# Kernel optimization log

Measured on AMD Instinct MI355X. Metric: run time of the kernel, lower is better.

## Reference

```python
import jax, jax.numpy as jnp
import numpy as np
from jax import lax

RHO = 1.0
L = 50

def _pbc_index(rho=RHO, L=L):
    # S = {(m,n) | |mn| <= rho*L//2, |m|<=L//2, |n|<=L//2}; rho*L//2 == 25.0 here
    thr = (rho * L) // 2
    idx = [(m, n)
           for m in range(-L // 2, L // 2 + 1)
           for n in range(-L // 2, L // 2 + 1)
           if abs(m * n) <= thr]
    return np.asarray(idx, dtype=np.int32)  # [T, 2], T = 449


def setup_inputs() -> dict:
    key = jax.random.key(0)
    k1, k2, k3, k4 = jax.random.split(key, 4)
    B, S, Nmodes = 8, 16384, 2
    T = _pbc_index().shape[0]  # 449
    return {
        "E_real": jax.random.normal(k1, (B, S, Nmodes), dtype=jnp.float32),
        "E_imag": jax.random.normal(k2, (B, S, Nmodes), dtype=jnp.float32),
        "C_real": jax.random.normal(k3, (4, T), dtype=jnp.float32) * 0.01,
        "C_imag": jax.random.normal(k4, (4, T), dtype=jnp.float32) * 0.01,
    }


def reference(E_real, E_imag, C_real, C_imag):
    idx = _pbc_index()
    m = jnp.asarray(idx[:, 0])
    n = jnp.asarray(idx[:, 1])
    E = E_real + 1j * E_imag                 # [B, S, 2] complex64
    C = (C_real + 1j * C_imag)[0]            # task_info=None -> row 0, [T]

    # O_k,i = E_k,i + sum_{m,n} (E_{k+n,i} E*_{k+m+n,i} + E_{k+n,-i} E*_{k+m+n,-i}) E_{k+m,i} C_{m,n}
    def body(acc, term):
        mi, ni, ci = term
        A = jnp.roll(E, ni, axis=-2) * jnp.conj(jnp.roll(E, mi + ni, axis=-2))
        A = A + jnp.roll(A, 1, axis=-1)      # cross-polarization term (Nmodes=2)
        return acc + A * jnp.roll(E, mi, axis=-2) * ci, None

    acc, _ = lax.scan(body, jnp.zeros_like(E), (m, n, C))
    Eo = E + acc                             # P = 1 (task_info=None), sqrt(P)**3 = 1
    return Eo[..., L:-L, :]                  # drop overlaps: [B, S-2L, 2]
```

## Files before the change

kernel.cpp:

```cpp
#include <hip/hip_runtime.h>


typedef float v2f __attribute__((ext_vector_type(2)));
typedef float v4f __attribute__((ext_vector_type(4)));

#define S_LEN 16384
#define SOUT  16284
#define BLK   512
#define NOUT  256
#define NE    356
#define NE2   178
#define ND    307
#define ND_AL 308
#define NDP   154

constexpr int LIMS[26] = {25,25,12,8,6,5,4,3,3,2,2,2,2,
                          1,1,1,1,1,1,1,1,1,1,1,1,1};
constexpr int TS[51] = {
      0,  3,  6,  9, 12, 15, 18, 21, 24, 27, 30, 33, 36,
     39, 44, 49, 54, 59, 66, 73, 82, 93,106,123,148,199,
    250,301,326,343,356,367,376,383,390,395,400,405,410,
    413,416,419,422,425,428,431,434,437,440,443,446};

template<int M>
__device__ __forceinline__ void convM(
    const float2* __restrict__ sDm, const v4f* __restrict__ sEp,
    int o0, const float* __restrict__ Cr0, const float* __restrict__ Ci0,
    float4& acc)
{
    constexpr int lim = LIMS[M];
    constexpr int tp  = TS[25 + M];
    constexpr int tn  = TS[25 - M];
    constexpr int A   = 25 + lim;

    v2f SxP0 = {0.f,0.f}, SyP0 = {0.f,0.f}, SxP1 = {0.f,0.f}, SyP1 = {0.f,0.f};
    v2f SxN0 = {0.f,0.f}, SyN0 = {0.f,0.f}, SxN1 = {0.f,0.f}, SyN1 = {0.f,0.f};

#define TAP(dconst, dd)                                                     \
    {                                                                       \
        const int d_ = (dconst);                                            \
        if (A - d_ >= 0 && A - d_ <= 2*lim) {                               \
            const float cx = Cr0[tp + A - d_], cy = Ci0[tp + A - d_];       \
            SxP0 += cx * (dd);  SyP0 += cy * (dd);                          \
        }                                                                   \
        if (A + 1 - d_ >= 0 && A + 1 - d_ <= 2*lim) {                       \
            const float cx = Cr0[tp + A+1-d_], cy = Ci0[tp + A+1-d_];       \
            SxP1 += cx * (dd);  SyP1 += cy * (dd);                          \
        }                                                                   \
        if (A + M - d_ >= 0 && A + M - d_ <= 2*lim) {                       \
            const float cx = Cr0[tn + A+M-d_], cy = Ci0[tn + A+M-d_];       \
            SxN0 += cx * (dd);  SyN0 += cy * (dd);                          \
        }                                                                   \
        if (A + M + 1 - d_ >= 0 && A + M + 1 - d_ <= 2*lim) {               \
            const float cx = Cr0[tn + A+M+1-d_], cy = Ci0[tn + A+M+1-d_];   \
            SxN1 += cx * (dd);  SyN1 += cy * (dd);                          \
        }                                                                   \
    }

    if constexpr (M < 2*lim + 4) {
        constexpr int dlo = (25 - lim) & ~1;
        constexpr int dhi = 26 + lim + M;
        constexpr int NP  = (dhi - dlo) / 2 + 1;
        #pragma unroll
        for (int p = 0; p < NP; ++p) {
            const int d0 = dlo + 2*p;
            v4f w = *reinterpret_cast<const v4f*>(&sDm[o0 + d0]);
            TAP(d0,     w.xy)
            TAP(d0 + 1, w.zw)
        }
    } else {
        {
            constexpr int dlo = (25 - lim) & ~1;
            constexpr int dhi = 26 + lim;
            constexpr int NP  = (dhi - dlo) / 2 + 1;
            #pragma unroll
            for (int p = 0; p < NP; ++p) {
                const int d0 = dlo + 2*p;
                v4f w = *reinterpret_cast<const v4f*>(&sDm[o0 + d0]);
                #pragma unroll
                for (int e = 0; e < 2; ++e) {
                    const int d = d0 + e;
                    const v2f dd = e ? w.zw : w.xy;
                    if (A - d >= 0 && A - d <= 2*lim) {
                        const float cx = Cr0[tp + A - d], cy = Ci0[tp + A - d];
                        SxP0 += cx * dd;  SyP0 += cy * dd;
                    }
                    if (A + 1 - d >= 0 && A + 1 - d <= 2*lim) {
                        const float cx = Cr0[tp + A+1-d], cy = Ci0[tp + A+1-d];
                        SxP1 += cx * dd;  SyP1 += cy * dd;
                    }
                }
            }
        }
        {
            constexpr int dlo = (25 + M - lim) & ~1;
            constexpr int dhi = 26 + M + lim;
            constexpr int NP  = (dhi - dlo) / 2 + 1;
            #pragma unroll
            for (int p = 0; p < NP; ++p) {
                const int d0 = dlo + 2*p;
                v4f w = *reinterpret_cast<const v4f*>(&sDm[o0 + d0]);
                #pragma unroll
                for (int e = 0; e < 2; ++e) {
                    const int d = d0 + e;
                    const v2f dd = e ? w.zw : w.xy;
                    if (A + M - d >= 0 && A + M - d <= 2*lim) {
                        const float cx = Cr0[tn + A+M-d], cy = Ci0[tn + A+M-d];
                        SxN0 += cx * dd;  SyN0 += cy * dd;
                    }
                    if (A + M + 1 - d >= 0 && A + M + 1 - d <= 2*lim) {
                        const float cx = Cr0[tn + A+M+1-d], cy = Ci0[tn + A+M+1-d];
                        SxN1 += cx * dd;  SyN1 += cy * dd;
                    }
                }
            }
        }
    }
#undef TAP

    const float s0pr = SxP0.x - SyP0.y, s0pi = SxP0.y + SyP0.x;
    const float s1pr = SxP1.x - SyP1.y, s1pi = SxP1.y + SyP1.x;
    const float s0nr = SxN0.x + SyN0.y, s0ni = SyN0.x - SxN0.y;
    const float s1nr = SxN1.x + SyN1.y, s1ni = SyN1.x - SxN1.y;

    const int t = o0 >> 1;
    v4f ep0, ep1, en0, en1;
    if constexpr ((M & 1) == 0) {
        ep0 = sEp[t + (50 - M)/2];
        ep1 = sEp[t + (50 - M)/2 + NE2];
        en0 = sEp[t + (50 + M)/2];
        en1 = sEp[t + (50 + M)/2 + NE2];
    } else {
        ep0 = sEp[t + (49 - M)/2 + NE2];
        ep1 = sEp[t + (51 - M)/2];
        en0 = sEp[t + (49 + M)/2 + NE2];
        en1 = sEp[t + (51 + M)/2];
    }
    acc.x += s0pr*ep0.x - s0pi*ep0.y + s0nr*en0.x - s0ni*en0.y;
    acc.y += s0pr*ep0.z - s0pi*ep0.w + s0nr*en0.z - s0ni*en0.w;
    acc.z += s1pr*ep1.x - s1pi*ep1.y + s1nr*en1.x - s1ni*en1.y;
    acc.w += s1pr*ep1.z - s1pi*ep1.w + s1nr*en1.z - s1ni*en1.w;
}

__device__ __forceinline__ void conv0(
    const float* __restrict__ sD0p, const v4f* __restrict__ sEp,
    int o0, const float* __restrict__ Cr0, const float* __restrict__ Ci0,
    float4& acc)
{
    v2f s0 = {0.f, 0.f}, s1 = {0.f, 0.f};
    #pragma unroll
    for (int p = 0; p < 13; ++p) {
        const int d0 = 4*p;
        v4f w = *reinterpret_cast<const v4f*>(&sD0p[o0 + d0]);
        #pragma unroll
        for (int e = 0; e < 4; ++e) {
            const int d = d0 + e;
            const float dv = (e == 0) ? w.x : (e == 1) ? w.y : (e == 2) ? w.z : w.w;
            if (50 - d >= 0) {
                v2f cv = { Cr0[199 + 50 - d], Ci0[199 + 50 - d] };
                s0 += dv * cv;
            }
            if (51 - d >= 0 && 51 - d <= 50) {
                v2f cv = { Cr0[199 + 51 - d], Ci0[199 + 51 - d] };
                s1 += dv * cv;
            }
        }
    }
    const int t = o0 >> 1;
    v4f e0 = sEp[t + 25];
    v4f e1 = sEp[t + 25 + NE2];
    acc.x += s0.x*e0.x - s0.y*e0.y;
    acc.y += s0.x*e0.z - s0.y*e0.w;
    acc.z += s1.x*e1.x - s1.y*e1.y;
    acc.w += s1.x*e1.z - s1.y*e1.w;
}

__global__ __launch_bounds__(BLK, 4) void pbc_kernel(
    const float* __restrict__ Er, const float* __restrict__ Ei,
    const float* __restrict__ Cr, const float* __restrict__ Ci,
    float* __restrict__ out)
{
    __shared__ __align__(16) v4f    sEp[NE];
    __shared__ __align__(16) float2 sD[25][ND_AL];
    __shared__ __align__(16) float  sD0[ND_AL];
    __shared__ __align__(16) float4 sAcc[4][128];

    const int b   = blockIdx.y;
    const int k0  = blockIdx.x * NOUT;
    const int tid = threadIdx.x;

    const float* erb = Er + (size_t)b * (S_LEN * 2);
    const float* eib = Ei + (size_t)b * (S_LEN * 2);
    if (tid < NE2) {
        const int i  = tid;
        const int kg = k0 + 2 * i;
        v4f rr = {0.f,0.f,0.f,0.f}, ii = {0.f,0.f,0.f,0.f};
        if (kg < S_LEN) {
            rr = *reinterpret_cast<const v4f*>(erb + 2 * kg);
            ii = *reinterpret_cast<const v4f*>(eib + 2 * kg);
        }
        sEp[i]       = (v4f){rr.x, ii.x, rr.y, ii.y};
        sEp[i + NE2] = (v4f){rr.z, ii.z, rr.w, ii.w};
    }
    __syncthreads();

    if (tid < NDP) {
        const int xp = tid;
        v4f a0 = sEp[xp + 12 + NE2];
        v4f a1 = sEp[xp + 13];
        float d0 = a0.x*a0.x + a0.y*a0.y + a0.z*a0.z + a0.w*a0.w;
        float d1 = a1.x*a1.x + a1.y*a1.y + a1.z*a1.z + a1.w*a1.w;
        *reinterpret_cast<float2*>(&sD0[2 * xp]) = make_float2(d0, d1);
    }
    for (int idx = tid; idx < 25 * NDP; idx += BLK) {
        const int m1 = idx / NDP;
        const int xp = idx - m1 * NDP;
        const int m  = m1 + 1;
        v4f a0 = sEp[xp + 12 + NE2];
        v4f a1 = sEp[xp + 13];
        const int sb  = 2 * xp + 25 - m;
        const int ib0 = (sb >> 1) + (sb & 1) * NE2;
        const int sb1 = sb + 1;
        const int ib1 = (sb1 >> 1) + (sb1 & 1) * NE2;
        v4f b0 = sEp[ib0], b1 = sEp[ib1];
        float gr0 = a0.x*b0.x + a0.y*b0.y + a0.z*b0.z + a0.w*b0.w;
        float gi0 = a0.y*b0.x - a0.x*b0.y + a0.w*b0.z - a0.z*b0.w;
        float gr1 = a1.x*b1.x + a1.y*b1.y + a1.z*b1.z + a1.w*b1.w;
        float gi1 = a1.y*b1.x - a1.x*b1.y + a1.w*b1.z - a1.z*b1.w;
        *reinterpret_cast<v4f*>(&sD[m1][2 * xp]) = (v4f){gr0, gi0, gr1, gi1};
    }
    __syncthreads();

    const int g  = tid >> 7;
    const int t  = tid & 127;
    const int o0 = 2 * t;

    float4 acc = make_float4(0.f, 0.f, 0.f, 0.f);
    if (g == 0) {
        convM<1>(sD[0],   sEp, o0, Cr, Ci, acc);
        convM<13>(sD[12], sEp, o0, Cr, Ci, acc);
        convM<14>(sD[13], sEp, o0, Cr, Ci, acc);
        convM<15>(sD[14], sEp, o0, Cr, Ci, acc);
        convM<16>(sD[15], sEp, o0, Cr, Ci, acc);
        convM<17>(sD[16], sEp, o0, Cr, Ci, acc);
    } else if (g == 1) {
        convM<2>(sD[1],   sEp, o0, Cr, Ci, acc);
        convM<4>(sD[3],   sEp, o0, Cr, Ci, acc);
        convM<7>(sD[6],   sEp, o0, Cr, Ci, acc);
        convM<9>(sD[8],   sEp, o0, Cr, Ci, acc);
        convM<18>(sD[17], sEp, o0, Cr, Ci, acc);
        convM<19>(sD[18], sEp, o0, Cr, Ci, acc);
    } else if (g == 2) {
        conv0(sD0, sEp, o0, Cr, Ci, acc);
        convM<3>(sD[2],   sEp, o0, Cr, Ci, acc);
        convM<8>(sD[7],   sEp, o0, Cr, Ci, acc);
        convM<10>(sD[9],  sEp, o0, Cr, Ci, acc);
        convM<12>(sD[11], sEp, o0, Cr, Ci, acc);
        convM<20>(sD[19], sEp, o0, Cr, Ci, acc);
    } else {
        convM<5>(sD[4],   sEp, o0, Cr, Ci, acc);
        convM<6>(sD[5],   sEp, o0, Cr, Ci, acc);
        convM<11>(sD[10], sEp, o0, Cr, Ci, acc);
        convM<21>(sD[20], sEp, o0, Cr, Ci, acc);
        convM<22>(sD[21], sEp, o0, Cr, Ci, acc);
        convM<23>(sD[22], sEp, o0, Cr, Ci, acc);
        convM<24>(sD[23], sEp, o0, Cr, Ci, acc);
        convM<25>(sD[24], sEp, o0, Cr, Ci, acc);
    }
    sAcc[g][t] = acc;
    __syncthreads();

    if (tid < 128) {
        const int tt = tid;
        const int oo = 2 * tt;
        const int ko = k0 + oo;
        if (ko < SOUT) {
            float4 p0 = sAcc[0][tt], p1 = sAcc[1][tt];
            float4 p2 = sAcc[2][tt], p3 = sAcc[3][tt];
            v4f e0 = sEp[tt + 25];
            v4f e1 = sEp[tt + 25 + NE2];
            float4 o;
            o.x = e0.x + p0.x + p1.x + p2.x + p3.x;
            o.y = e0.z + p0.y + p1.y + p2.y + p3.y;
            o.z = e1.x + p0.z + p1.z + p2.z + p3.z;
            o.w = e1.z + p0.w + p1.w + p2.w + p3.w;
            *reinterpret_cast<float4*>(out + ((size_t)b * SOUT + ko) * 2) = o;
        }
    }
}

extern "C" void kernel_launch(void* const* d_in, const int* in_sizes, int n_in,
                              void* d_out, int out_size, void* d_ws, size_t ws_size,
                              hipStream_t stream) {
    const float* Er = (const float*)d_in[0];
    const float* Ei = (const float*)d_in[1];
    const float* Cr = (const float*)d_in[2];
    const float* Ci = (const float*)d_in[3];
    float* out = (float*)d_out;

    dim3 grid((SOUT + NOUT - 1) / NOUT, 8);
    pbc_kernel<<<grid, BLK, 0, stream>>>(Er, Ei, Cr, Ci, out);
}
```

Measured before the change: 17.34 us.

## Register-block four outputs per thread, store intermediates as bf16, regroup warps

Each thread now computes four consecutive outputs instead of two, so every shared-memory load of the intermediate products feeds four accumulators. The per-m intermediate products are packed to bf16 pairs, which halves LDS footprint and read bandwidth. The m-values are redistributed over eight 64-thread groups, with a seven-way cross-group reduction at the end. This trades lower LDS traffic for more registers per thread and reduced precision of the intermediate terms, which may affect accuracy.

```diff
diff --git a/kernel.cpp b/kernel.cpp
--- a/kernel.cpp
+++ b/kernel.cpp
@@ -22,157 +22,156 @@
     250,301,326,343,356,367,376,383,390,395,400,405,410,
     413,416,419,422,425,428,431,434,437,440,443,446};
 
+__device__ __forceinline__ uint32_t pack_bf(float re, float im) {
+    uint32_t r;
+    asm("v_cvt_pk_bf16_f32 %0, %1, %2" : "=v"(r) : "v"(re), "v"(im));
+    return r;
+}
+__device__ __forceinline__ v2f unpack_bf(uint32_t u) {
+    union { uint32_t i; float f; } lo, hi;
+    lo.i = u << 16;
+    hi.i = u & 0xFFFF0000u;
+    return (v2f){lo.f, hi.f};
+}
+
 template<int M>
-__device__ __forceinline__ void convM(
-    const float2* __restrict__ sDm, const v4f* __restrict__ sEp,
+__device__ __forceinline__ void convM4(
+    const uint32_t* __restrict__ sDm, const v4f* __restrict__ sEp,
     int o0, const float* __restrict__ Cr0, const float* __restrict__ Ci0,
-    float4& acc)
+    float4& acc01, float4& acc23)
 {
     constexpr int lim = LIMS[M];
     constexpr int tp  = TS[25 + M];
     constexpr int tn  = TS[25 - M];
     constexpr int A   = 25 + lim;
 
-    v2f SxP0 = {0.f,0.f}, SyP0 = {0.f,0.f}, SxP1 = {0.f,0.f}, SyP1 = {0.f,0.f};
-    v2f SxN0 = {0.f,0.f}, SyN0 = {0.f,0.f}, SxN1 = {0.f,0.f}, SyN1 = {0.f,0.f};
-
-#define TAP(dconst, dd)                                                     \
+    v2f SxP[4] = {{0.f,0.f},{0.f,0.f},{0.f,0.f},{0.f,0.f}};
+    v2f SyP[4] = {{0.f,0.f},{0.f,0.f},{0.f,0.f},{0.f,0.f}};
+    v2f SxN[4] = {{0.f,0.f},{0.f,0.f},{0.f,0.f},{0.f,0.f}};
+    v2f SyN[4] = {{0.f,0.f},{0.f,0.f},{0.f,0.f},{0.f,0.f}};
+
+#define TAP4(d_, dd)                                                        \
+    { _Pragma("unroll")                                                     \
+      for (int r = 0; r < 4; ++r) {                                         \
+        if (A + r - (d_) >= 0 && A + r - (d_) <= 2*lim) {                   \
+            const float cx = Cr0[tp + A + r - (d_)];                        \
+            const float cy = Ci0[tp + A + r - (d_)];                        \
+            SxP[r] += cx * (dd);  SyP[r] += cy * (dd);                      \
+        }                                                                   \
+        if (A + M + r - (d_) >= 0 && A + M + r - (d_) <= 2*lim) {           \
+            const float cx = Cr0[tn + A + M + r - (d_)];                    \
+            const float cy = Ci0[tn + A + M + r - (d_)];                    \
+            SxN[r] += cx * (dd);  SyN[r] += cy * (dd);                      \
+        }                                                                   \
+      } }
+#define TAP4P(d_, dd)                                                       \
+    { _Pragma("unroll")                                                     \
+      for (int r = 0; r < 4; ++r) {                                         \
+        if (A + r - (d_) >= 0 && A + r - (d_) <= 2*lim) {                   \
+            const float cx = Cr0[tp + A + r - (d_)];                        \
+            const float cy = Ci0[tp + A + r - (d_)];                        \
+            SxP[r] += cx * (dd);  SyP[r] += cy * (dd);                      \
+        }                                                                   \
+      } }
+#define TAP4N(d_, dd)                                                       \
+    { _Pragma("unroll")                                                     \
+      for (int r = 0; r < 4; ++r) {                                         \
+        if (A + M + r - (d_) >= 0 && A + M + r - (d_) <= 2*lim) {           \
+            const float cx = Cr0[tn + A + M + r - (d_)];                    \
+            const float cy = Ci0[tn + A + M + r - (d_)];                    \
+            SxN[r] += cx * (dd);  SyN[r] += cy * (dd);                      \
+        }                                                                   \
+      } }
+#define QUAD(d0_, TAPM)                                                     \
     {                                                                       \
-        const int d_ = (dconst);                                            \
-        if (A - d_ >= 0 && A - d_ <= 2*lim) {                               \
-            const float cx = Cr0[tp + A - d_], cy = Ci0[tp + A - d_];       \
-            SxP0 += cx * (dd);  SyP0 += cy * (dd);                          \
-        }                                                                   \
-        if (A + 1 - d_ >= 0 && A + 1 - d_ <= 2*lim) {                       \
-            const float cx = Cr0[tp + A+1-d_], cy = Ci0[tp + A+1-d_];       \
-            SxP1 += cx * (dd);  SyP1 += cy * (dd);                          \
-        }                                                                   \
-        if (A + M - d_ >= 0 && A + M - d_ <= 2*lim) {                       \
-            const float cx = Cr0[tn + A+M-d_], cy = Ci0[tn + A+M-d_];       \
-            SxN0 += cx * (dd);  SyN0 += cy * (dd);                          \
-        }                                                                   \
-        if (A + M + 1 - d_ >= 0 && A + M + 1 - d_ <= 2*lim) {               \
-            const float cx = Cr0[tn + A+M+1-d_], cy = Ci0[tn + A+M+1-d_];   \
-            SxN1 += cx * (dd);  SyN1 += cy * (dd);                          \
-        }                                                                   \
+        uint4 u = *reinterpret_cast<const uint4*>(&sDm[o0 + (d0_)]);        \
+        TAPM((d0_) + 0, unpack_bf(u.x))                                     \
+        TAPM((d0_) + 1, unpack_bf(u.y))                                     \
+        TAPM((d0_) + 2, unpack_bf(u.z))                                     \
+        TAPM((d0_) + 3, unpack_bf(u.w))                                     \
     }
 
     if constexpr (M < 2*lim + 4) {
-        constexpr int dlo = (25 - lim) & ~1;
-        constexpr int dhi = 26 + lim + M;
-        constexpr int NP  = (dhi - dlo) / 2 + 1;
+        constexpr int dlo = (25 - lim) & ~3;
+        constexpr int dhi = 28 + lim + M;
+        constexpr int NQ  = (dhi - dlo) / 4 + 1;
         #pragma unroll
-        for (int p = 0; p < NP; ++p) {
-            const int d0 = dlo + 2*p;
-            v4f w = *reinterpret_cast<const v4f*>(&sDm[o0 + d0]);
-            TAP(d0,     w.xy)
-            TAP(d0 + 1, w.zw)
-        }
+        for (int q = 0; q < NQ; ++q)
+            QUAD(dlo + 4*q, TAP4)
     } else {
         {
-            constexpr int dlo = (25 - lim) & ~1;
-            constexpr int dhi = 26 + lim;
-            constexpr int NP  = (dhi - dlo) / 2 + 1;
+            constexpr int dlo = (25 - lim) & ~3;
+            constexpr int dhi = 28 + lim;
+            constexpr int NQ  = (dhi - dlo) / 4 + 1;
             #pragma unroll
-            for (int p = 0; p < NP; ++p) {
-                const int d0 = dlo + 2*p;
-                v4f w = *reinterpret_cast<const v4f*>(&sDm[o0 + d0]);
-                #pragma unroll
-                for (int e = 0; e < 2; ++e) {
-                    const int d = d0 + e;
-                    const v2f dd = e ? w.zw : w.xy;
-                    if (A - d >= 0 && A - d <= 2*lim) {
-                        const float cx = Cr0[tp + A - d], cy = Ci0[tp + A - d];
-                        SxP0 += cx * dd;  SyP0 += cy * dd;
-                    }
-                    if (A + 1 - d >= 0 && A + 1 - d <= 2*lim) {
-                        const float cx = Cr0[tp + A+1-d], cy = Ci0[tp + A+1-d];
-                        SxP1 += cx * dd;  SyP1 += cy * dd;
-                    }
-                }
-            }
+            for (int q = 0; q < NQ; ++q)
+                QUAD(dlo + 4*q, TAP4P)
         }
         {
-            constexpr int dlo = (25 + M - lim) & ~1;
-            constexpr int dhi = 26 + M + lim;
-            constexpr int NP  = (dhi - dlo) / 2 + 1;
+            constexpr int dlo = (25 + M - lim) & ~3;
+            constexpr int dhi = 28 + M + lim;
+            constexpr int NQ  = (dhi - dlo) / 4 + 1;
             #pragma unroll
-            for (int p = 0; p < NP; ++p) {
-                const int d0 = dlo + 2*p;
-                v4f w = *reinterpret_cast<const v4f*>(&sDm[o0 + d0]);
-                #pragma unroll
-                for (int e = 0; e < 2; ++e) {
-                    const int d = d0 + e;
-                    const v2f dd = e ? w.zw : w.xy;
-                    if (A + M - d >= 0 && A + M - d <= 2*lim) {
-                        const float cx = Cr0[tn + A+M-d], cy = Ci0[tn + A+M-d];
-                        SxN0 += cx * dd;  SyN0 += cy * dd;
-                    }
-                    if (A + M + 1 - d >= 0 && A + M + 1 - d <= 2*lim) {
-                        const float cx = Cr0[tn + A+M+1-d], cy = Ci0[tn + A+M+1-d];
-                        SxN1 += cx * dd;  SyN1 += cy * dd;
-                    }
-                }
-            }
-        }
-    }
-#undef TAP
-
-    const float s0pr = SxP0.x - SyP0.y, s0pi = SxP0.y + SyP0.x;
-    const float s1pr = SxP1.x - SyP1.y, s1pi = SxP1.y + SyP1.x;
-    const float s0nr = SxN0.x + SyN0.y, s0ni = SyN0.x - SxN0.y;
-    const float s1nr = SxN1.x + SyN1.y, s1ni = SyN1.x - SxN1.y;
-
-    const int t = o0 >> 1;
-    v4f ep0, ep1, en0, en1;
-    if constexpr ((M & 1) == 0) {
-        ep0 = sEp[t + (50 - M)/2];
-        ep1 = sEp[t + (50 - M)/2 + NE2];
-        en0 = sEp[t + (50 + M)/2];
-        en1 = sEp[t + (50 + M)/2 + NE2];
-    } else {
-        ep0 = sEp[t + (49 - M)/2 + NE2];
-        ep1 = sEp[t + (51 - M)/2];
-        en0 = sEp[t + (49 + M)/2 + NE2];
-        en1 = sEp[t + (51 + M)/2];
-    }
-    acc.x += s0pr*ep0.x - s0pi*ep0.y + s0nr*en0.x - s0ni*en0.y;
-    acc.y += s0pr*ep0.z - s0pi*ep0.w + s0nr*en0.z - s0ni*en0.w;
-    acc.z += s1pr*ep1.x - s1pi*ep1.y + s1nr*en1.x - s1ni*en1.y;
-    acc.w += s1pr*ep1.z - s1pi*ep1.w + s1nr*en1.z - s1ni*en1.w;
-}
-
-__device__ __forceinline__ void conv0(
+            for (int q = 0; q < NQ; ++q)
+                QUAD(dlo + 4*q, TAP4N)
+        }
+    }
+#undef QUAD
+#undef TAP4
+#undef TAP4P
+#undef TAP4N
+
+    #pragma unroll
+    for (int r = 0; r < 4; ++r) {
+        const float spr = SxP[r].x - SyP[r].y, spi = SxP[r].y + SyP[r].x;
+        const float snr = SxN[r].x + SyN[r].y, sni = SyN[r].x - SxN[r].y;
+        const int sp = o0 + 50 + r - M;
+        const int sn = o0 + 50 + r + M;
+        v4f ep = sEp[(sp >> 1) + ((sp & 1) ? NE2 : 0)];
+        v4f en = sEp[(sn >> 1) + ((sn & 1) ? NE2 : 0)];
+        const float c0 = spr*ep.x - spi*ep.y + snr*en.x - sni*en.y;
+        const float c1 = spr*ep.z - spi*ep.w + snr*en.z - sni*en.w;
+        if      (r == 0) { acc01.x += c0; acc01.y += c1; }
+        else if (r == 1) { acc01.z += c0; acc01.w += c1; }
+        else if (r == 2) { acc23.x += c0; acc23.y += c1; }
+        else             { acc23.z += c0; acc23.w += c1; }
+    }
+}
+
+__device__ __forceinline__ void conv04(
     const float* __restrict__ sD0p, const v4f* __restrict__ sEp,
     int o0, const float* __restrict__ Cr0, const float* __restrict__ Ci0,
-    float4& acc)
+    float4& acc01, float4& acc23)
 {
-    v2f s0 = {0.f, 0.f}, s1 = {0.f, 0.f};
+    v2f s[4] = {{0.f,0.f},{0.f,0.f},{0.f,0.f},{0.f,0.f}};
     #pragma unroll
-    for (int p = 0; p < 13; ++p) {
-        const int d0 = 4*p;
+    for (int q = 0; q < 14; ++q) {
+        const int d0 = 4*q;
         v4f w = *reinterpret_cast<const v4f*>(&sD0p[o0 + d0]);
         #pragma unroll
         for (int e = 0; e < 4; ++e) {
             const int d = d0 + e;
-            const float dv = (e == 0) ? w.x : (e == 1) ? w.y : (e == 2) ? w.z : w.w;
-            if (50 - d >= 0) {
-                v2f cv = { Cr0[199 + 50 - d], Ci0[199 + 50 - d] };
-                s0 += dv * cv;
+            const float dv = (e==0) ? w.x : (e==1) ? w.y : (e==2) ? w.z : w.w;
+            #pragma unroll
+            for (int r = 0; r < 4; ++r) {
+                if (50 + r - d >= 0 && 50 + r - d <= 50) {
+                    v2f cv = { Cr0[199 + 50 + r - d], Ci0[199 + 50 + r - d] };
+                    s[r] += dv * cv;
+                }
             }
-            if (51 - d >= 0 && 51 - d <= 50) {
-                v2f cv = { Cr0[199 + 51 - d], Ci0[199 + 51 - d] };
-                s1 += dv * cv;
-            }
-        }
-    }
-    const int t = o0 >> 1;
-    v4f e0 = sEp[t + 25];
-    v4f e1 = sEp[t + 25 + NE2];
-    acc.x += s0.x*e0.x - s0.y*e0.y;
-    acc.y += s0.x*e0.z - s0.y*e0.w;
-    acc.z += s1.x*e1.x - s1.y*e1.y;
-    acc.w += s1.x*e1.z - s1.y*e1.w;
+        }
+    }
+    #pragma unroll
+    for (int r = 0; r < 4; ++r) {
+        const int sp = o0 + 50 + r;
+        v4f e = sEp[(sp >> 1) + ((sp & 1) ? NE2 : 0)];
+        const float c0 = s[r].x*e.x - s[r].y*e.y;
+        const float c1 = s[r].x*e.z - s[r].y*e.w;
+        if      (r == 0) { acc01.x += c0; acc01.y += c1; }
+        else if (r == 1) { acc01.z += c0; acc01.w += c1; }
+        else if (r == 2) { acc23.x += c0; acc23.y += c1; }
+        else             { acc23.z += c0; acc23.w += c1; }
+    }
 }
 
 __global__ __launch_bounds__(BLK, 4) void pbc_kernel(
@@ -180,10 +179,10 @@
     const float* __restrict__ Cr, const float* __restrict__ Ci,
     float* __restrict__ out)
 {
-    __shared__ __align__(16) v4f    sEp[NE];
-    __shared__ __align__(16) float2 sD[25][ND_AL];
-    __shared__ __align__(16) float  sD0[ND_AL];
-    __shared__ __align__(16) float4 sAcc[4][128];
+    __shared__ __align__(16) v4f      sEp[NE];
+    __shared__ __align__(16) uint32_t sDbf[25 * ND_AL];
+    __shared__ __align__(16) float    sD0[ND_AL];
+    __shared__ __align__(16) float4   sAcc[7][64][2];
 
     const int b   = blockIdx.y;
     const int k0  = blockIdx.x * NOUT;
@@ -227,64 +226,84 @@
         float gi0 = a0.y*b0.x - a0.x*b0.y + a0.w*b0.z - a0.z*b0.w;
         float gr1 = a1.x*b1.x + a1.y*b1.y + a1.z*b1.z + a1.w*b1.w;
         float gi1 = a1.y*b1.x - a1.x*b1.y + a1.w*b1.z - a1.z*b1.w;
-        *reinterpret_cast<v4f*>(&sD[m1][2 * xp]) = (v4f){gr0, gi0, gr1, gi1};
+        *reinterpret_cast<uint2*>(&sDbf[m1 * ND_AL + 2 * xp]) =
+            make_uint2(pack_bf(gr0, gi0), pack_bf(gr1, gi1));
     }
     __syncthreads();
 
-    const int g  = tid >> 7;
-    const int t  = tid & 127;
-    const int o0 = 2 * t;
-
-    float4 acc = make_float4(0.f, 0.f, 0.f, 0.f);
+    const int g  = tid >> 6;
+    const int t  = tid & 63;
+    const int o0 = 4 * t;
+
+    float4 acc01 = make_float4(0.f,0.f,0.f,0.f);
+    float4 acc23 = make_float4(0.f,0.f,0.f,0.f);
+#define DM(mm) (sDbf + ((mm) - 1) * ND_AL)
     if (g == 0) {
-        convM<1>(sD[0],   sEp, o0, Cr, Ci, acc);
-        convM<13>(sD[12], sEp, o0, Cr, Ci, acc);
-        convM<14>(sD[13], sEp, o0, Cr, Ci, acc);
-        convM<15>(sD[14], sEp, o0, Cr, Ci, acc);
-        convM<16>(sD[15], sEp, o0, Cr, Ci, acc);
-        convM<17>(sD[16], sEp, o0, Cr, Ci, acc);
+        conv04(sD0, sEp, o0, Cr, Ci, acc01, acc23);
+        convM4<1>(DM(1), sEp, o0, Cr, Ci, acc01, acc23);
     } else if (g == 1) {
-        convM<2>(sD[1],   sEp, o0, Cr, Ci, acc);
-        convM<4>(sD[3],   sEp, o0, Cr, Ci, acc);
-        convM<7>(sD[6],   sEp, o0, Cr, Ci, acc);
-        convM<9>(sD[8],   sEp, o0, Cr, Ci, acc);
-        convM<18>(sD[17], sEp, o0, Cr, Ci, acc);
-        convM<19>(sD[18], sEp, o0, Cr, Ci, acc);
+        convM4<2>(DM(2), sEp, o0, Cr, Ci, acc01, acc23);
+        convM4<3>(DM(3), sEp, o0, Cr, Ci, acc01, acc23);
+        convM4<4>(DM(4), sEp, o0, Cr, Ci, acc01, acc23);
     } else if (g == 2) {
-        conv0(sD0, sEp, o0, Cr, Ci, acc);
-        convM<3>(sD[2],   sEp, o0, Cr, Ci, acc);
-        convM<8>(sD[7],   sEp, o0, Cr, Ci, acc);
-        convM<10>(sD[9],  sEp, o0, Cr, Ci, acc);
-        convM<12>(sD[11], sEp, o0, Cr, Ci, acc);
-        convM<20>(sD[19], sEp, o0, Cr, Ci, acc);
+        convM4<5>(DM(5), sEp, o0, Cr, Ci, acc01, acc23);
+        convM4<6>(DM(6), sEp, o0, Cr, Ci, acc01, acc23);
+        convM4<7>(DM(7), sEp, o0, Cr, Ci, acc01, acc23);
+    } else if (g == 3) {
+        convM4<8>(DM(8), sEp, o0, Cr, Ci, acc01, acc23);
+        convM4<9>(DM(9), sEp, o0, Cr, Ci, acc01, acc23);
+        convM4<10>(DM(10), sEp, o0, Cr, Ci, acc01, acc23);
+    } else if (g == 4) {
+        convM4<11>(DM(11), sEp, o0, Cr, Ci, acc01, acc23);
+        convM4<12>(DM(12), sEp, o0, Cr, Ci, acc01, acc23);
+        convM4<13>(DM(13), sEp, o0, Cr, Ci, acc01, acc23);
+        convM4<14>(DM(14), sEp, o0, Cr, Ci, acc01, acc23);
+    } else if (g == 5) {
+        convM4<15>(DM(15), sEp, o0, Cr, Ci, acc01, acc23);
+        convM4<16>(DM(16), sEp, o0, Cr, Ci, acc01, acc23);
+        convM4<17>(DM(17), sEp, o0, Cr, Ci, acc01, acc23);
+        convM4<18>(DM(18), sEp, o0, Cr, Ci, acc01, acc23);
+    } else if (g == 6) {
+        convM4<19>(DM(19), sEp, o0, Cr, Ci, acc01, acc23);
+        convM4<20>(DM(20), sEp, o0, Cr, Ci, acc01, acc23);
+        convM4<21>(DM(21), sEp, o0, Cr, Ci, acc01, acc23);
+        convM4<22>(DM(22), sEp, o0, Cr, Ci, acc01, acc23);
     } else {
-        convM<5>(sD[4],   sEp, o0, Cr, Ci, acc);
-        convM<6>(sD[5],   sEp, o0, Cr, Ci, acc);
-        convM<11>(sD[10], sEp, o0, Cr, Ci, acc);
-        convM<21>(sD[20], sEp, o0, Cr, Ci, acc);
-        convM<22>(sD[21], sEp, o0, Cr, Ci, acc);
-        convM<23>(sD[22], sEp, o0, Cr, Ci, acc);
-        convM<24>(sD[23], sEp, o0, Cr, Ci, acc);
-        convM<25>(sD[24], sEp, o0, Cr, Ci, acc);
-    }
-    sAcc[g][t] = acc;
+        convM4<23>(DM(23), sEp, o0, Cr, Ci, acc01, acc23);
+        convM4<24>(DM(24), sEp, o0, Cr, Ci, acc01, acc23);
+        convM4<25>(DM(25), sEp, o0, Cr, Ci, acc01, acc23);
+    }
+#undef DM
+    if (g > 0) {
+        sAcc[g - 1][t][0] = acc01;
+        sAcc[g - 1][t][1] = acc23;
+    }
     __syncthreads();
 
-    if (tid < 128) {
+    if (tid < 64) {
         const int tt = tid;
-        const int oo = 2 * tt;
+        const int oo = 4 * tt;
         const int ko = k0 + oo;
         if (ko < SOUT) {
-            float4 p0 = sAcc[0][tt], p1 = sAcc[1][tt];
-            float4 p2 = sAcc[2][tt], p3 = sAcc[3][tt];
-            v4f e0 = sEp[tt + 25];
-            v4f e1 = sEp[tt + 25 + NE2];
-            float4 o;
-            o.x = e0.x + p0.x + p1.x + p2.x + p3.x;
-            o.y = e0.z + p0.y + p1.y + p2.y + p3.y;
-            o.z = e1.x + p0.z + p1.z + p2.z + p3.z;
-            o.w = e1.z + p0.w + p1.w + p2.w + p3.w;
-            *reinterpret_cast<float4*>(out + ((size_t)b * SOUT + ko) * 2) = o;
+            float4 a01 = acc01, a23 = acc23;
+            #pragma unroll
+            for (int i = 0; i < 7; ++i) {
+                float4 p0 = sAcc[i][tt][0], p1 = sAcc[i][tt][1];
+                a01.x += p0.x; a01.y += p0.y; a01.z += p0.z; a01.w += p0.w;
+                a23.x += p1.x; a23.y += p1.y; a23.z += p1.z; a23.w += p1.w;
+            }
+            v4f e0 = sEp[2*tt + 25];
+            v4f e1 = sEp[2*tt + 25 + NE2];
+            v4f e2 = sEp[2*tt + 26];
+            v4f e3 = sEp[2*tt + 26 + NE2];
+            float4 o0v, o1v;
+            o0v.x = e0.x + a01.x;  o0v.y = e0.z + a01.y;
+            o0v.z = e1.x + a01.z;  o0v.w = e1.z + a01.w;
+            o1v.x = e2.x + a23.x;  o1v.y = e2.z + a23.y;
+            o1v.z = e3.x + a23.z;  o1v.w = e3.z + a23.w;
+            float* dst = out + ((size_t)b * SOUT + ko) * 2;
+            *reinterpret_cast<float4*>(dst)     = o0v;
+            *reinterpret_cast<float4*>(dst + 4) = o1v;
         }
     }
 }
```

Measured after the change: 16.08 us. -7.3%, faster.
